# Optimization experiments

Measured on AMD Instinct MI355X. Metric: run time of the kernel, lower is better.

## Reference

```python
import jax, jax.numpy as jnp
import numpy as np

TOKEN_BITS = 10
CODEBOOK_SIZE = 2 ** TOKEN_BITS
COMMITMENT_COST = 0.25
ENT_WEIGHT = 0.1
ENT_TEMP = 0.01
ENT_GAMMA = 1.0
EPS = 1e-5


def _make_codebook():
    bits_to_indices = 2 ** np.arange(TOKEN_BITS, dtype=np.int64)  # [c]
    all_codes = np.arange(CODEBOOK_SIZE, dtype=np.int64)  # [n]
    bits = ((all_codes[:, None] & bits_to_indices) != 0).astype(np.float32)
    return jnp.asarray(bits * 2.0 - 1.0)  # [n, c] in {-1, +1}


def setup_inputs() -> dict:
    key = jax.random.key(0)
    z = jax.random.normal(key, (64, 10, 32, 32), dtype=jnp.float32)  # [b, c, h, w]
    codebook = _make_codebook()  # [1024, 10]
    return {"z": z, "codebook": codebook}


def reference(z, codebook):
    # b c h w -> b h w c
    zc = jnp.transpose(z, (0, 2, 3, 1))
    # strategy == 'default': sign quantization to {-1, +1}
    z_hard = jnp.where(zc > 0.0, 1.0, -1.0).astype(zc.dtype)

    # bit-pack indices (bits represented by sign)
    bits_to_indices = (2 ** jnp.arange(TOKEN_BITS, dtype=jnp.int32))  # [c]
    min_encoding_indices = jnp.sum((zc > 0.0).astype(jnp.int32) * bits_to_indices, axis=-1)  # [b, h, w]

    # entropy loss (ent_strategy == 'default', training mode)
    d = -2.0 * jnp.einsum('bhwc,nc->bhwn', zc, codebook)
    affinity = (-d).reshape(-1, CODEBOOK_SIZE) / ENT_TEMP  # [bhw, n]
    probs = jax.nn.softmax(affinity, axis=-1)
    log_probs = jax.nn.log_softmax(affinity + EPS, axis=-1)
    per_sample_entropy = -jnp.mean(jnp.sum(probs * log_probs, axis=-1))
    avg_probs = jnp.mean(probs, axis=0)  # [n]
    avg_entropy = -jnp.sum(avg_probs * jnp.log(avg_probs + EPS)) * ENT_GAMMA
    entropy_loss = ENT_WEIGHT * (per_sample_entropy - avg_entropy)

    # straight-through estimator
    z_q = zc + jax.lax.stop_gradient(z_hard - zc)
    commitment_loss = COMMITMENT_COST * jnp.mean((jax.lax.stop_gradient(z_q) - zc) ** 2)
    loss = commitment_loss + entropy_loss

    z_q_out = jnp.transpose(z_q, (0, 3, 1, 2))  # b h w c -> b c h w
    return (z_q_out, loss, commitment_loss, entropy_loss,
            per_sample_entropy, avg_entropy, min_encoding_indices)
```

## Files before the change

kernel.cpp:

```cpp
#include <hip/hip_runtime.h>
#include <math.h>

#define NPIX    65536
#define NELEM   655360
#define NCODE   1024
#define CSTRIDE 1024
#define BSTRIDE 10240
#define NCOPY   16

#define SOFT_T 0.22f


__global__ void __launch_bounds__(256)
k_pixel(const float* __restrict__ z,
        float* __restrict__ zq,
        float* __restrict__ out_idx,
        float* __restrict__ ws) {
    __shared__ float hist[NCODE];
    __shared__ uint2 s_e[256 * 11];
    __shared__ float2 red[256];

    int tid = threadIdx.x;
    for (int i = tid; i < NCODE; i += 256) hist[i] = 0.f;
    __syncthreads();

    int p = blockIdx.x * 256 + tid;
    int b = p >> 10;
    int hw = p & 1023;
    const float* zp = z  + b * BSTRIDE + hw;
    float*       qp = zq + b * BSTRIDE + hw;
    uint2* et = &s_e[tid * 11];

    int idx = 0, k = 0;
    float commit = 0.f;
    float Z = 1.f, W = 0.f;
#pragma unroll
    for (int c = 0; c < 10; ++c) {
        float x = zp[c * CSTRIDE];
        float h = (x > 0.f) ? 1.f : -1.f;
        qp[c * CSTRIDE] = h;
        float d = h - x;
        commit = fmaf(d, d, commit);
        if (x > 0.f) idx |= (1 << c);
        float a = fabsf(x);
        float t = -400.f * a;
        float e = __expf(t);
        float r = e / (1.f + e);
        Z *= (1.f + e);
        W = fmaf(t, r, W);
        if (a < SOFT_T) {
            uint2 u; u.x = __float_as_uint(a); u.y = 1u << c;
            et[k] = u; ++k;
        }
    }
    out_idx[p] = (float)idx;
    float invZ = 1.f / Z;
    float plogp = W - logf(Z);

    int nsub = 1 << k;
    atomicAdd(&hist[idx], invZ);
    float s = 0.f;
    int gray = 0;
    unsigned cmask = 0;
    uint2 cur = et[0];
    for (int m = 1; m < nsub; ++m) {
        int bit  = __ffs(m) - 1;     (void)bit;
        int nbit = __ffs(m + 1) - 1;
        uint2 nxt = et[nbit];
        int bm = 1 << (__ffs(m) - 1);
        gray ^= bm;
        float a = __uint_as_float(cur.x);
        s += (gray & bm) ? a : -a;
        cmask ^= cur.y;
        atomicAdd(&hist[idx ^ cmask], __expf(-400.f * s) * invZ);
        cur = nxt;
    }

    red[tid] = make_float2(plogp, commit);
    __syncthreads();
    for (int st = 128; st > 0; st >>= 1) {
        if (tid < st) {
            red[tid].x += red[tid + st].x;
            red[tid].y += red[tid + st].y;
        }
        __syncthreads();
    }
    if (tid == 0) {
        atomicAdd(&ws[1], red[0].x);
        atomicAdd(&ws[0], red[0].y);
    }

    float* hcopy = ws + 2 + (size_t)(blockIdx.x & (NCOPY - 1)) * NCODE;
    for (int i = tid; i < NCODE; i += 256) {
        float hv = hist[i];
        if (hv != 0.f) atomicAdd(&hcopy[i], hv);
    }
}

__global__ void __launch_bounds__(1024)
k_final(const float* __restrict__ ws, float* __restrict__ out_sc) {
    __shared__ float red[1024];
    int t = threadIdx.x;
    float a = 0.f;
#pragma unroll
    for (int j = 0; j < NCOPY; ++j) a += ws[2 + j * NCODE + t];
    a *= (1.f / 65536.f);
    red[t] = -a * logf(a + 1e-5f);
    __syncthreads();
    for (int s = 512; s > 0; s >>= 1) {
        if (t < s) red[t] += red[t + s];
        __syncthreads();
    }
    if (t == 0) {
        float avg_entropy = red[0];
        float pse = -ws[1] * (1.f / 65536.f);
        float cl  = 0.25f * ws[0] * (1.f / (float)NELEM);
        float el  = 0.1f * (pse - avg_entropy);
        out_sc[0] = cl + el;
        out_sc[1] = cl;
        out_sc[2] = el;
        out_sc[3] = pse;
        out_sc[4] = avg_entropy;
    }
}

extern "C" void kernel_launch(void* const* d_in, const int* in_sizes, int n_in,
                              void* d_out, int out_size, void* d_ws, size_t ws_size,
                              hipStream_t stream) {
    const float* z = (const float*)d_in[0];
    float* out = (float*)d_out;
    float* ws = (float*)d_ws;

    hipMemsetAsync(ws, 0, (2 + NCOPY * NCODE) * sizeof(float), stream);
    k_pixel<<<NPIX / 256, 256, 0, stream>>>(z, out, out + NELEM + 5, ws);
    k_final<<<1, 1024, 0, stream>>>(ws, out + NELEM);
}
```

Baseline: 75.76 us.

## Split per-pixel subset enumeration across four lanes and drop global atomics

```diff
diff --git a/kernel.cpp b/kernel.cpp
--- a/kernel.cpp
+++ b/kernel.cpp
@@ -6,9 +6,15 @@
 #define NCODE   1024
 #define CSTRIDE 1024
 #define BSTRIDE 10240
-#define NCOPY   16
+#define NBLK    1024
+#define NHB     32
 
 #define SOFT_T 0.22f
+
+#define WS_HIST 0
+#define WS_PLP  (NBLK * NCODE)
+#define WS_COM  (WS_PLP + NBLK)
+#define WS_ENT  (WS_COM + NBLK)
 
 
 __global__ void __launch_bounds__(256)
@@ -17,66 +23,84 @@
         float* __restrict__ out_idx,
         float* __restrict__ ws) {
     __shared__ float hist[NCODE];
-    __shared__ uint2 s_e[256 * 11];
+    __shared__ uint2 s_e[64 * 11];
     __shared__ float2 red[256];
 
     int tid = threadIdx.x;
     for (int i = tid; i < NCODE; i += 256) hist[i] = 0.f;
+
+    float commit = 0.f;
+    {
+        int i0 = blockIdx.x * 256 + tid;
+        float x = z[i0];
+        float h = (x > 0.f) ? 1.f : -1.f;
+        zq[i0] = h; float d = h - x; commit = fmaf(d, d, commit);
+        int i1 = i0 + 262144;
+        x = z[i1]; h = (x > 0.f) ? 1.f : -1.f;
+        zq[i1] = h; d = h - x; commit = fmaf(d, d, commit);
+        int i2 = i1 + 262144;
+        if (i2 < NELEM) {
+            x = z[i2]; h = (x > 0.f) ? 1.f : -1.f;
+            zq[i2] = h; d = h - x; commit = fmaf(d, d, commit);
+        }
+    }
     __syncthreads();
 
-    int p = blockIdx.x * 256 + tid;
+    int p   = blockIdx.x * 64 + (tid >> 2);
+    int sub = tid & 3;
     int b = p >> 10;
     int hw = p & 1023;
-    const float* zp = z  + b * BSTRIDE + hw;
-    float*       qp = zq + b * BSTRIDE + hw;
-    uint2* et = &s_e[tid * 11];
+    const float* zp = z + b * BSTRIDE + hw;
+    uint2* et = &s_e[(tid >> 2) * 11];
 
     int idx = 0, k = 0;
-    float commit = 0.f;
     float Z = 1.f, W = 0.f;
 #pragma unroll
     for (int c = 0; c < 10; ++c) {
         float x = zp[c * CSTRIDE];
-        float h = (x > 0.f) ? 1.f : -1.f;
-        qp[c * CSTRIDE] = h;
-        float d = h - x;
-        commit = fmaf(d, d, commit);
         if (x > 0.f) idx |= (1 << c);
         float a = fabsf(x);
         float t = -400.f * a;
         float e = __expf(t);
-        float r = e / (1.f + e);
         Z *= (1.f + e);
-        W = fmaf(t, r, W);
+        W = fmaf(t, e / (1.f + e), W);
         if (a < SOFT_T) {
             uint2 u; u.x = __float_as_uint(a); u.y = 1u << c;
             et[k] = u; ++k;
         }
     }
-    out_idx[p] = (float)idx;
+    if (sub == 0) out_idx[p] = (float)idx;
     float invZ = 1.f / Z;
     float plogp = W - logf(Z);
 
-    int nsub = 1 << k;
-    atomicAdd(&hist[idx], invZ);
-    float s = 0.f;
-    int gray = 0;
-    unsigned cmask = 0;
-    uint2 cur = et[0];
-    for (int m = 1; m < nsub; ++m) {
-        int bit  = __ffs(m) - 1;     (void)bit;
-        int nbit = __ffs(m + 1) - 1;
-        uint2 nxt = et[nbit];
-        int bm = 1 << (__ffs(m) - 1);
-        gray ^= bm;
-        float a = __uint_as_float(cur.x);
-        s += (gray & bm) ? a : -a;
-        cmask ^= cur.y;
-        atomicAdd(&hist[idx ^ cmask], __expf(-400.f * s) * invZ);
-        cur = nxt;
+    float s0 = 0.f; unsigned cm0 = 0;
+    bool active; int nIter;
+    if (k >= 2) {
+        active = true;
+        nIter = 1 << (k - 2);
+        if (sub & 1) { uint2 u = et[k - 1]; s0 += __uint_as_float(u.x); cm0 ^= u.y; }
+        if (sub & 2) { uint2 u = et[k - 2]; s0 += __uint_as_float(u.x); cm0 ^= u.y; }
+    } else {
+        active = sub < (1 << k);
+        nIter = 1;
+        if (k == 1 && sub == 1) { uint2 u = et[0]; s0 = __uint_as_float(u.x); cm0 = u.y; }
+    }
+    if (active) {
+        atomicAdd(&hist[idx ^ cm0], __expf(-400.f * s0) * invZ);
+        int gray = 0; float s = s0; unsigned cmask = cm0;
+        for (int m = 1; m < nIter; ++m) {
+            int bit = __ffs(m) - 1;
+            uint2 u = et[bit];
+            int bm = 1 << bit;
+            gray ^= bm;
+            float a = __uint_as_float(u.x);
+            s += (gray & bm) ? a : -a;
+            cmask ^= u.y;
+            atomicAdd(&hist[idx ^ cmask], __expf(-400.f * s) * invZ);
+        }
     }
 
-    red[tid] = make_float2(plogp, commit);
+    red[tid] = make_float2((sub == 0) ? plogp : 0.f, commit);
     __syncthreads();
     for (int st = 128; st > 0; st >>= 1) {
         if (tid < st) {
@@ -86,35 +110,61 @@
         __syncthreads();
     }
     if (tid == 0) {
-        atomicAdd(&ws[1], red[0].x);
-        atomicAdd(&ws[0], red[0].y);
+        ws[WS_PLP + blockIdx.x] = red[0].x;
+        ws[WS_COM + blockIdx.x] = red[0].y;
     }
 
-    float* hcopy = ws + 2 + (size_t)(blockIdx.x & (NCOPY - 1)) * NCODE;
-    for (int i = tid; i < NCODE; i += 256) {
-        float hv = hist[i];
-        if (hv != 0.f) atomicAdd(&hcopy[i], hv);
+    float* hc = ws + WS_HIST + (size_t)blockIdx.x * NCODE;
+    for (int i = tid; i < NCODE; i += 256) hc[i] = hist[i];
+}
+
+__global__ void __launch_bounds__(256)
+k_hist(const float* __restrict__ ws, float* __restrict__ ws_w) {
+    __shared__ float sh[256];
+    int bin0 = blockIdx.x * 32;
+    int bin = threadIdx.x & 31;
+    int grp = threadIdx.x >> 5;
+    float acc = 0.f;
+    for (int c = grp; c < NBLK; c += 8)
+        acc += ws[WS_HIST + (size_t)c * NCODE + bin0 + bin];
+    sh[threadIdx.x] = acc;
+    __syncthreads();
+    if (threadIdx.x < 32) {
+        float a = sh[bin];
+#pragma unroll
+        for (int g = 1; g < 8; ++g) a += sh[g * 32 + bin];
+        a *= (1.f / 65536.f);
+        float ent = -a * logf(a + 1e-5f);
+        for (int off = 16; off > 0; off >>= 1)
+            ent += __shfl_down(ent, off, 32);
+        if (bin == 0) ws_w[WS_ENT + blockIdx.x] = ent;
     }
 }
 
-__global__ void __launch_bounds__(1024)
-k_final(const float* __restrict__ ws, float* __restrict__ out_sc) {
-    __shared__ float red[1024];
+__global__ void __launch_bounds__(256)
+k_scalars(const float* __restrict__ ws, float* __restrict__ out_sc) {
+    __shared__ float2 red[256];
     int t = threadIdx.x;
-    float a = 0.f;
+    float plp = 0.f, com = 0.f;
 #pragma unroll
-    for (int j = 0; j < NCOPY; ++j) a += ws[2 + j * NCODE + t];
-    a *= (1.f / 65536.f);
-    red[t] = -a * logf(a + 1e-5f);
+    for (int j = 0; j < 4; ++j) {
+        plp += ws[WS_PLP + t + j * 256];
+        com += ws[WS_COM + t + j * 256];
+    }
+    red[t] = make_float2(plp, com);
     __syncthreads();
-    for (int s = 512; s > 0; s >>= 1) {
-        if (t < s) red[t] += red[t + s];
+    for (int st = 128; st > 0; st >>= 1) {
+        if (t < st) {
+            red[t].x += red[t + st].x;
+            red[t].y += red[t + st].y;
+        }
         __syncthreads();
     }
     if (t == 0) {
-        float avg_entropy = red[0];
-        float pse = -ws[1] * (1.f / 65536.f);
-        float cl  = 0.25f * ws[0] * (1.f / (float)NELEM);
+        float avg_entropy = 0.f;
+        for (int g = 0; g < NHB; ++g) avg_entropy += ws[WS_ENT + g];
+        float pse = -red[0].x * (1.f / 65536.f);
+        float cl  = 0.25f * red[0].y * (1.f / (float)NELEM);
         float el  = 0.1f * (pse - avg_entropy);
         out_sc[0] = cl + el;
         out_sc[1] = cl;
@@ -131,7 +181,7 @@
     float* out = (float*)d_out;
     float* ws = (float*)d_ws;
 
-    hipMemsetAsync(ws, 0, (2 + NCOPY * NCODE) * sizeof(float), stream);
-    k_pixel<<<NPIX / 256, 256, 0, stream>>>(z, out, out + NELEM + 5, ws);
-    k_final<<<1, 1024, 0, stream>>>(ws, out + NELEM);
+    k_pixel<<<NBLK, 256, 0, stream>>>(z, out, out + NELEM + 5, ws);
+    k_hist<<<NHB, 256, 0, stream>>>(ws, ws);
+    k_scalars<<<1, 256, 0, stream>>>(ws, out + NELEM);
 }
```

New measurement: 106.9 us. 41.1% more time.

## Replace global histogram atomics with per-block partials and a parallel reduction kernel

Applied to the files above, without the earlier changes.

```diff
diff --git a/kernel.cpp b/kernel.cpp
--- a/kernel.cpp
+++ b/kernel.cpp
@@ -6,9 +6,15 @@
 #define NCODE   1024
 #define CSTRIDE 1024
 #define BSTRIDE 10240
-#define NCOPY   16
+#define NBLK    256
+#define NHB     16
 
 #define SOFT_T 0.22f
+
+#define WS_HIST 0
+#define WS_PLP  (NBLK * NCODE)
+#define WS_COM  (WS_PLP + NBLK)
+#define WS_ENT  (WS_COM + NBLK)
 
 
 __global__ void __launch_bounds__(256)
@@ -45,17 +51,17 @@
         float a = fabsf(x);
         float t = -400.f * a;
         float e = __expf(t);
-        float r = e / (1.f + e);
-        Z *= (1.f + e);
-        W = fmaf(t, r, W);
+        float op = 1.f + e;
+        Z *= op;
+        W = fmaf(t, e * __builtin_amdgcn_rcpf(op), W);
         if (a < SOFT_T) {
             uint2 u; u.x = __float_as_uint(a); u.y = 1u << c;
             et[k] = u; ++k;
         }
     }
     out_idx[p] = (float)idx;
-    float invZ = 1.f / Z;
-    float plogp = W - logf(Z);
+    float invZ = __builtin_amdgcn_rcpf(Z);
+    float plogp = W - __logf(Z);
 
     int nsub = 1 << k;
     atomicAdd(&hist[idx], invZ);
@@ -64,7 +70,6 @@
     unsigned cmask = 0;
     uint2 cur = et[0];
     for (int m = 1; m < nsub; ++m) {
-        int bit  = __ffs(m) - 1;     (void)bit;
         int nbit = __ffs(m + 1) - 1;
         uint2 nxt = et[nbit];
         int bm = 1 << (__ffs(m) - 1);
@@ -86,35 +91,60 @@
         __syncthreads();
     }
     if (tid == 0) {
-        atomicAdd(&ws[1], red[0].x);
-        atomicAdd(&ws[0], red[0].y);
+        ws[WS_PLP + blockIdx.x] = red[0].x;
+        ws[WS_COM + blockIdx.x] = red[0].y;
     }
 
-    float* hcopy = ws + 2 + (size_t)(blockIdx.x & (NCOPY - 1)) * NCODE;
-    for (int i = tid; i < NCODE; i += 256) {
-        float hv = hist[i];
-        if (hv != 0.f) atomicAdd(&hcopy[i], hv);
+    float4* hc = (float4*)(ws + WS_HIST + (size_t)blockIdx.x * NCODE);
+    float4* hs = (float4*)hist;
+    hc[tid] = hs[tid];
+}
+
+__global__ void __launch_bounds__(1024)
+k_hist(const float* __restrict__ ws, float* __restrict__ ws_w) {
+    __shared__ float sh[16 * 64];
+    int t = threadIdx.x;
+    int lane = t & 63;
+    int w = t >> 6;
+    int bin = blockIdx.x * 64 + lane;
+    float acc = 0.f;
+#pragma unroll 4
+    for (int c = w; c < NBLK; c += 16)
+        acc += ws[WS_HIST + (size_t)c * NCODE + bin];
+    sh[w * 64 + lane] = acc;
+    __syncthreads();
+    if (t < 64) {
+        float a = sh[lane];
+#pragma unroll
+        for (int g = 1; g < 16; ++g) a += sh[g * 64 + lane];
+        a *= (1.f / 65536.f);
+        float ent = -a * __logf(a + 1e-5f);
+#pragma unroll
+        for (int off = 32; off > 0; off >>= 1)
+            ent += __shfl_down(ent, off, 64);
+        if (lane == 0) ws_w[WS_ENT + blockIdx.x] = ent;
     }
 }
 
-__global__ void __launch_bounds__(1024)
-k_final(const float* __restrict__ ws, float* __restrict__ out_sc) {
-    __shared__ float red[1024];
+__global__ void __launch_bounds__(256)
+k_scalars(const float* __restrict__ ws, float* __restrict__ out_sc) {
+    __shared__ float2 red[256];
     int t = threadIdx.x;
-    float a = 0.f;
-#pragma unroll
-    for (int j = 0; j < NCOPY; ++j) a += ws[2 + j * NCODE + t];
-    a *= (1.f / 65536.f);
-    red[t] = -a * logf(a + 1e-5f);
+    red[t] = make_float2(ws[WS_PLP + t], ws[WS_COM + t]);
     __syncthreads();
-    for (int s = 512; s > 0; s >>= 1) {
-        if (t < s) red[t] += red[t + s];
+    for (int st = 128; st > 0; st >>= 1) {
+        if (t < st) {
+            red[t].x += red[t + st].x;
+            red[t].y += red[t + st].y;
+        }
         __syncthreads();
     }
     if (t == 0) {
-        float avg_entropy = red[0];
-        float pse = -ws[1] * (1.f / 65536.f);
-        float cl  = 0.25f * ws[0] * (1.f / (float)NELEM);
+        float avg_entropy = 0.f;
+#pragma unroll
+        for (int g = 0; g < NHB; ++g) avg_entropy += ws[WS_ENT + g];
+        float pse = -red[0].x * (1.f / 65536.f);
+        float cl  = 0.25f * red[0].y * (1.f / (float)NELEM);
         float el  = 0.1f * (pse - avg_entropy);
         out_sc[0] = cl + el;
         out_sc[1] = cl;
@@ -131,7 +161,7 @@
     float* out = (float*)d_out;
     float* ws = (float*)d_ws;
 
-    hipMemsetAsync(ws, 0, (2 + NCOPY * NCODE) * sizeof(float), stream);
-    k_pixel<<<NPIX / 256, 256, 0, stream>>>(z, out, out + NELEM + 5, ws);
-    k_final<<<1, 1024, 0, stream>>>(ws, out + NELEM);
+    k_pixel<<<NBLK, 256, 0, stream>>>(z, out, out + NELEM + 5, ws);
+    k_hist<<<NHB, 1024, 0, stream>>>(ws, ws);
+    k_scalars<<<1, 256, 0, stream>>>(ws, out + NELEM);
 }
```

Result: faster. 73.33 us (median of 2 runs) (-3.2%).
